# Optimization experiments

Hardware: AMD Instinct MI355X
Metric: run time of the kernel (lower is better)

Reference implementation:

```python
import jax, jax.numpy as jnp
import numpy as np

# model constants (match init_kwargs)
B, T, D = 2, 2048, 2048          # batch, seq_len, d_model (= d_in = d_out)
H, G = 32, 8                     # num_heads, num_kv_groups
HD = D // H                      # head_dim = 64
GROUP = H // G                   # 4 query heads per KV group
ROPE_BASE = 10000.0


def _apply_rope(x):
    # x: (b, heads, t, hd); rotate-half RoPE over absolute positions 0..t-1
    t = x.shape[2]
    half = HD // 2
    inv_freq = 1.0 / (ROPE_BASE ** (jnp.arange(half, dtype=jnp.float32) * 2.0 / HD))
    ang = jnp.arange(t, dtype=jnp.float32)[:, None] * inv_freq[None, :]   # (t, half)
    cos, sin = jnp.cos(ang), jnp.sin(ang)
    x1, x2 = x[..., :half], x[..., half:]
    out = jnp.concatenate([x1 * cos - x2 * sin, x2 * cos + x1 * sin], axis=-1)
    return out.astype(x.dtype)


def setup_inputs() -> dict:
    key = jax.random.key(0)
    kx, kq, kk, kv, ko = jax.random.split(key, 5)
    scale = 0.02
    x = jax.random.normal(kx, (B, T, D), dtype=jnp.float32)
    # linear weights stored as (in, out) so y = x @ W
    Wq = jax.random.normal(kq, (D, D), dtype=jnp.float32) * scale
    Wk = jax.random.normal(kk, (D, G * HD), dtype=jnp.float32) * scale
    Wv = jax.random.normal(kv, (D, G * HD), dtype=jnp.float32) * scale
    Wo = jax.random.normal(ko, (D, D), dtype=jnp.float32) * scale
    return {"x": x, "Wq": Wq, "Wk": Wk, "Wv": Wv, "Wo": Wo}


def reference(x, Wq, Wk, Wv, Wo):
    b, t, _ = x.shape
    q = (x @ Wq).reshape(b, t, H, HD).transpose(0, 2, 1, 3)   # (b, H, t, hd)
    k = (x @ Wk).reshape(b, t, G, HD).transpose(0, 2, 1, 3)   # (b, G, t, hd)
    v = (x @ Wv).reshape(b, t, G, HD).transpose(0, 2, 1, 3)
    q = _apply_rope(q)
    k = _apply_rope(k)
    # GQA: physically duplicate K/V per query-head group (repeat_interleave)
    k = jnp.repeat(k, GROUP, axis=1)                          # (b, H, t, hd)
    v = jnp.repeat(v, GROUP, axis=1)
    scores = jnp.einsum('bhqd,bhkd->bhqk', q, k)              # (b, H, t, t)
    causal = jnp.triu(jnp.ones((t, t), dtype=bool), k=1)
    scores = jnp.where(causal, -jnp.inf, scores)
    attn = jax.nn.softmax(scores / jnp.sqrt(jnp.float32(HD)), axis=-1)
    ctx = jnp.einsum('bhqk,bhkd->bhqd', attn, v)              # (b, H, t, hd)
    # faithful to source: transpose(-2, -1) then reshape (NOT the usual (b,t,H,hd) order)
    ctx = jnp.swapaxes(ctx, -2, -1).reshape(b, t, D)
    return ctx @ Wo
```

## Files before the change

kernel.cpp:

```cpp
#include <hip/hip_runtime.h>

typedef unsigned short u16;
typedef unsigned int u32;
typedef __bf16 bf16x8 __attribute__((ext_vector_type(8)));
typedef float f32x4 __attribute__((ext_vector_type(4)));
typedef u16 u16x8 __attribute__((ext_vector_type(8)));
typedef __attribute__((address_space(1))) const void gvoid;
typedef __attribute__((address_space(3))) void svoid;

#define T_SEQ 2048
#define NEG_INF (-__builtin_huge_valf())

__device__ __forceinline__ u16 f2bf(float f) {
  union { float f; unsigned u; } x; x.f = f;
  unsigned u = x.u;
  return (u16)((u + 0x7FFFu + ((u >> 16) & 1u)) >> 16);
}
__device__ __forceinline__ float bf2f(u16 h) {
  union { unsigned u; float f; } x; x.u = ((unsigned)h) << 16;
  return x.f;
}
__device__ __forceinline__ u32 pack_bf2(float lo, float hi) {
  u32 r;
  asm("v_cvt_pk_bf16_f32 %0, %1, %2" : "=v"(r) : "v"(lo), "v"(hi));
  return r;
}
__device__ __forceinline__ int swz16(int row, int col16) {
  int blk = (col16 >> 3) ^ (row & 7) ^ ((row >> 3) & 7);
  return row * 64 + ((blk & 7) << 3) + (col16 & 7);
}

__global__ __launch_bounds__(256) void cast_f32_bf16(const float* __restrict__ in,
                                                     u16* __restrict__ out, long n) {
  long i = ((long)blockIdx.x * 256 + threadIdx.x) * 4;
  if (i >= n) return;
  float4 v = *(const float4*)(in + i);
  ushort4 o;
  o.x = f2bf(v.x); o.y = f2bf(v.y); o.z = f2bf(v.z); o.w = f2bf(v.w);
  *(ushort4*)(out + i) = o;
}

__global__ __launch_bounds__(256) void transpose_cast(const float* __restrict__ W,
                                                      u16* __restrict__ WT, int K, int N) {
  __shared__ float tile[32][33];
  int nb = blockIdx.x * 32, kb = blockIdx.y * 32;
  int tx = threadIdx.x, ty = threadIdx.y;
  #pragma unroll
  for (int i = 0; i < 32; i += 8)
    tile[ty + i][tx] = W[(size_t)(kb + ty + i) * N + nb + tx];
  __syncthreads();
  #pragma unroll
  for (int i = 0; i < 32; i += 8)
    WT[(size_t)(nb + ty + i) * K + kb + tx] = f2bf(tile[tx][ty + i]);
}

__global__ __launch_bounds__(256) void rope_table_k(float2* __restrict__ tab) {
  int idx = blockIdx.x * 256 + threadIdx.x;
  int t = idx >> 5, d = idx & 31;
  float inv = powf(10000.0f, -(float)d / 32.0f);
  float ang = (float)t * inv;
  float s, c;
  sincosf(ang, &s, &c);
  tab[idx] = make_float2(c, s);
}

__global__ __launch_bounds__(256) void rope_apply_v(u16* __restrict__ X,
                                                    const float2* __restrict__ tab,
                                                    long total, int lsh) {
  long idx = (long)blockIdx.x * 256 + threadIdx.x;
  if (idx >= total) return;
  int row = (int)(idx >> lsh);
  int u = (int)(idx & ((1 << lsh) - 1));
  int h = u >> 2, d0 = (u & 3) << 3;
  int t = row & (T_SEQ - 1);
  int cols = 1 << (lsh + 4);
  u16* p = X + (size_t)row * cols + h * 64 + d0;
  u16x8 lo = *(u16x8*)p;
  u16x8 hi = *(u16x8*)(p + 32);
  const float4* tp = (const float4*)(tab + t * 32 + d0);
  float4 cs0 = tp[0], cs1 = tp[1], cs2 = tp[2], cs3 = tp[3];
  float cbuf[16];
  *(float4*)(cbuf) = cs0; *(float4*)(cbuf + 4) = cs1;
  *(float4*)(cbuf + 8) = cs2; *(float4*)(cbuf + 12) = cs3;
  u16x8 olo, ohi;
  #pragma unroll
  for (int e = 0; e < 8; ++e) {
    float c = cbuf[2 * e], s = cbuf[2 * e + 1];
    float x1 = bf2f(lo[e]), x2 = bf2f(hi[e]);
    olo[e] = f2bf(x1 * c - x2 * s);
    ohi[e] = f2bf(x2 * c + x1 * s);
  }
  *(u16x8*)p = olo;
  *(u16x8*)(p + 32) = ohi;
}

template<int OUT_F32>
__global__ __launch_bounds__(256) void gemm_bt(const u16* __restrict__ A,
                                               const u16* __restrict__ BT,
                                               void* __restrict__ Cout,
                                               int M, int N, int K) {
  __shared__ __align__(16) u16 As[128 * 64];
  __shared__ __align__(16) u16 Bs[128 * 64];
  const int tid = threadIdx.x;
  const int w = tid >> 6, lane = tid & 63;
  const int r16 = lane & 15, kg = lane >> 4;
  const size_t rowBase = (size_t)blockIdx.y * 128;
  const size_t colBase = (size_t)blockIdx.x * 128;
  const int wm = (w >> 1) * 64, wn = (w & 1) * 64;
  f32x4 acc[4][4] = {};

  const u16* Abase = A + (rowBase + w * 32 + (lane >> 3)) * (size_t)K + (lane & 7) * 8;
  const u16* Bbase = BT + (colBase + w * 32 + (lane >> 3)) * (size_t)K + (lane & 7) * 8;

  for (int k0 = 0; k0 < K; k0 += 64) {
    __syncthreads();
    #pragma unroll
    for (int i = 0; i < 4; ++i) {
      __builtin_amdgcn_global_load_lds((gvoid*)(Abase + (size_t)i * 8 * K + k0),
                                       (svoid*)(&As[(w * 32 + i * 8) * 64]), 16, 0, 0);
      __builtin_amdgcn_global_load_lds((gvoid*)(Bbase + (size_t)i * 8 * K + k0),
                                       (svoid*)(&Bs[(w * 32 + i * 8) * 64]), 16, 0, 0);
    }
    __syncthreads();
    #pragma unroll
    for (int kk = 0; kk < 2; ++kk) {
      bf16x8 af[4], bfv[4];
      #pragma unroll
      for (int mi = 0; mi < 4; ++mi)
        af[mi] = *(const bf16x8*)(&As[(wm + mi * 16 + r16) * 64 + kk * 32 + kg * 8]);
      #pragma unroll
      for (int ni = 0; ni < 4; ++ni)
        bfv[ni] = *(const bf16x8*)(&Bs[(wn + ni * 16 + r16) * 64 + kk * 32 + kg * 8]);
      __builtin_amdgcn_s_setprio(1);
      #pragma unroll
      for (int mi = 0; mi < 4; ++mi)
        #pragma unroll
        for (int ni = 0; ni < 4; ++ni)
          acc[mi][ni] = __builtin_amdgcn_mfma_f32_16x16x32_bf16(af[mi], bfv[ni], acc[mi][ni], 0, 0, 0);
      __builtin_amdgcn_s_setprio(0);
    }
  }

  #pragma unroll
  for (int mi = 0; mi < 4; ++mi)
    #pragma unroll
    for (int ni = 0; ni < 4; ++ni) {
      size_t row = rowBase + wm + mi * 16 + kg * 4;
      size_t col = colBase + wn + ni * 16 + r16;
      if (OUT_F32) {
        float* C = (float*)Cout;
        #pragma unroll
        for (int r = 0; r < 4; ++r) C[(row + r) * N + col] = acc[mi][ni][r];
      } else {
        u16* C = (u16*)Cout;
        #pragma unroll
        for (int r = 0; r < 4; ++r) C[(row + r) * N + col] = f2bf(acc[mi][ni][r]);
      }
    }
}

__global__ __launch_bounds__(256) void attn_fwd(const u16* __restrict__ Q,
                                                const u16* __restrict__ Kg,
                                                const u16* __restrict__ Vg,
                                                u16* __restrict__ ctxT) {
  const int bh = blockIdx.x, qt = blockIdx.y;
  const int b = bh >> 5, h = bh & 31, g = h >> 2;
  const int tid = threadIdx.x, w = tid >> 6, lane = tid & 63;
  const int r16 = lane & 15, kg = lane >> 4;
  const int qbase = qt * 128;
  const int wq = qbase + w * 32;

  const u16* Qp = Q + (size_t)b * T_SEQ * 2048 + (size_t)h * 64;
  const u16* Kp = Kg + (size_t)b * T_SEQ * 512 + (size_t)g * 64;
  const u16* Vp = Vg + (size_t)b * T_SEQ * 512 + (size_t)g * 64;

  __shared__ __align__(16) u16 Kt[64 * 64];
  __shared__ __align__(16) u16 Vt[64 * 64];

  bf16x8 qf[2][2];
  #pragma unroll
  for (int mi = 0; mi < 2; ++mi)
    #pragma unroll
    for (int ks = 0; ks < 2; ++ks)
      qf[mi][ks] = *(const bf16x8*)(Qp + (size_t)(wq + mi * 16 + r16) * 2048 + ks * 32 + kg * 8);

  f32x4 acc[4][2] = {};
  float m_i[2] = {NEG_INF, NEG_INF}, l_i[2] = {0.0f, 0.0f};
  const float SCALE = 0.18033688f;

  const int nkt = (qbase + 128) >> 6;
  const int srow = tid >> 3, sc8 = tid & 7;

  for (int kt = 0; kt < nkt; ++kt) {
    const int kvb = kt << 6;
    __syncthreads();
    #pragma unroll
    for (int p = 0; p < 2; ++p) {
      int row = p * 32 + srow;
      bf16x8 kv8 = *(const bf16x8*)(Kp + (size_t)(kvb + row) * 512 + sc8 * 8);
      *(bf16x8*)(&Kt[swz16(row, sc8 * 8)]) = kv8;
    }
    {
      bf16x8 v0 = *(const bf16x8*)(Vp + (size_t)(kvb + 2 * srow) * 512 + sc8 * 8);
      bf16x8 v1 = *(const bf16x8*)(Vp + (size_t)(kvb + 2 * srow + 1) * 512 + sc8 * 8);
      const u16* va = (const u16*)&v0;
      const u16* vb = (const u16*)&v1;
      #pragma unroll
      for (int j = 0; j < 8; ++j) {
        u32 wv = (u32)va[j] | ((u32)vb[j] << 16);
        *(u32*)(&Vt[swz16(sc8 * 8 + j, 2 * srow)]) = wv;
      }
    }
    __syncthreads();
    if (kvb > wq + 31) continue;

    f32x4 st[4][2] = {};
    #pragma unroll
    for (int ks = 0; ks < 2; ++ks) {
      bf16x8 kf[4];
      #pragma unroll
      for (int ni = 0; ni < 4; ++ni)
        kf[ni] = *(const bf16x8*)(&Kt[swz16(ni * 16 + r16, ks * 32 + kg * 8)]);
      __builtin_amdgcn_s_setprio(1);
      #pragma unroll
      for (int ni = 0; ni < 4; ++ni)
        #pragma unroll
        for (int mi = 0; mi < 2; ++mi)
          st[ni][mi] = __builtin_amdgcn_mfma_f32_16x16x32_bf16(kf[ni], qf[mi][ks], st[ni][mi], 0, 0, 0);
      __builtin_amdgcn_s_setprio(0);
    }

    u32 pkk[2][4][2];
    #pragma unroll
    for (int mi = 0; mi < 2; ++mi) {
      const int q = wq + mi * 16 + r16;
      float mx = NEG_INF;
      #pragma unroll
      for (int ni = 0; ni < 4; ++ni)
        #pragma unroll
        for (int r = 0; r < 4; ++r) {
          float v = st[ni][mi][r];
          int kv = kvb + ni * 16 + kg * 4 + r;
          v = (kv <= q) ? v : NEG_INF;
          st[ni][mi][r] = v;
          mx = fmaxf(mx, v);
        }
      mx = fmaxf(mx, __shfl_xor(mx, 16, 64));
      mx = fmaxf(mx, __shfl_xor(mx, 32, 64));
      float mnew = fmaxf(m_i[mi], mx);
      float alpha = exp2f((m_i[mi] - mnew) * SCALE);
      float nm = mnew * SCALE;
      m_i[mi] = mnew;
      float rs = 0.0f;
      #pragma unroll
      for (int ni = 0; ni < 4; ++ni) {
        float p0 = exp2f(fmaf(st[ni][mi][0], SCALE, -nm));
        float p1 = exp2f(fmaf(st[ni][mi][1], SCALE, -nm));
        float p2 = exp2f(fmaf(st[ni][mi][2], SCALE, -nm));
        float p3 = exp2f(fmaf(st[ni][mi][3], SCALE, -nm));
        rs += (p0 + p1) + (p2 + p3);
        pkk[mi][ni][0] = pack_bf2(p0, p1);
        pkk[mi][ni][1] = pack_bf2(p2, p3);
      }
      rs += __shfl_xor(rs, 16, 64);
      rs += __shfl_xor(rs, 32, 64);
      l_i[mi] = l_i[mi] * alpha + rs;
      #pragma unroll
      for (int di = 0; di < 4; ++di)
        #pragma unroll
        for (int r = 0; r < 4; ++r) acc[di][mi][r] *= alpha;
    }

    #pragma unroll
    for (int ks = 0; ks < 2; ++ks) {
      bf16x8 vfr[4];
      #pragma unroll
      for (int di = 0; di < 4; ++di)
        vfr[di] = *(const bf16x8*)(&Vt[swz16(di * 16 + r16, ks * 32 + kg * 8)]);
      const int s0 = ((kg & 1) * 2) * 16 + r16;
      const int s1 = s0 + 16;
      const bool hi = (kg >> 1) != 0;
      #pragma unroll
      for (int mi = 0; mi < 2; ++mi) {
        u32 a0 = __shfl(pkk[mi][2 * ks][0], s0, 64);
        u32 b0 = __shfl(pkk[mi][2 * ks + 1][0], s0, 64);
        u32 a1 = __shfl(pkk[mi][2 * ks][1], s0, 64);
        u32 b1 = __shfl(pkk[mi][2 * ks + 1][1], s0, 64);
        u32 a2 = __shfl(pkk[mi][2 * ks][0], s1, 64);
        u32 b2 = __shfl(pkk[mi][2 * ks + 1][0], s1, 64);
        u32 a3 = __shfl(pkk[mi][2 * ks][1], s1, 64);
        u32 b3 = __shfl(pkk[mi][2 * ks + 1][1], s1, 64);
        union { u32 u[4]; bf16x8 v; } pu;
        pu.u[0] = hi ? b0 : a0;
        pu.u[1] = hi ? b1 : a1;
        pu.u[2] = hi ? b2 : a2;
        pu.u[3] = hi ? b3 : a3;
        __builtin_amdgcn_s_setprio(1);
        #pragma unroll
        for (int di = 0; di < 4; ++di)
          acc[di][mi] = __builtin_amdgcn_mfma_f32_16x16x32_bf16(vfr[di], pu.v, acc[di][mi], 0, 0, 0);
        __builtin_amdgcn_s_setprio(0);
      }
    }
  }

  float inv[2] = {1.0f / l_i[0], 1.0f / l_i[1]};
  #pragma unroll
  for (int di = 0; di < 4; ++di)
    #pragma unroll
    for (int mi = 0; mi < 2; ++mi)
      #pragma unroll
      for (int r = 0; r < 4; ++r) {
        size_t row = (size_t)(b * 2048 + h * 64 + di * 16 + kg * 4 + r);
        ctxT[row * 2048 + wq + mi * 16 + r16] = f2bf(acc[di][mi][r] * inv[mi]);
      }
}

extern "C" void kernel_launch(void* const* d_in, const int* in_sizes, int n_in,
                              void* d_out, int out_size, void* d_ws, size_t ws_size,
                              hipStream_t stream) {
  const float* x  = (const float*)d_in[0];
  const float* Wq = (const float*)d_in[1];
  const float* Wk = (const float*)d_in[2];
  const float* Wv = (const float*)d_in[3];
  const float* Wo = (const float*)d_in[4];
  float* out = (float*)d_out;
  char* ws = (char*)d_ws;

  u16* xb   = (u16*)(ws);
  u16* Qb   = (u16*)(ws + 16777216);
  u16* Kb   = (u16*)(ws + 33554432);
  u16* Vb   = (u16*)(ws + 37748736);
  u16* ctxT = (u16*)(ws + 41943040);
  u16* WqT  = (u16*)(ws + 58720256);
  u16* WkT  = (u16*)(ws + 67108864);
  u16* WvT  = (u16*)(ws + 69206016);
  u16* WoT  = (u16*)(ws + 71303168);
  float2* tab = (float2*)(ws + 79691776);

  cast_f32_bf16<<<8192, 256, 0, stream>>>(x, xb, 8388608L);
  rope_table_k<<<256, 256, 0, stream>>>(tab);
  transpose_cast<<<dim3(64, 64), dim3(32, 8), 0, stream>>>(Wq, WqT, 2048, 2048);
  transpose_cast<<<dim3(16, 64), dim3(32, 8), 0, stream>>>(Wk, WkT, 2048, 512);
  transpose_cast<<<dim3(16, 64), dim3(32, 8), 0, stream>>>(Wv, WvT, 2048, 512);
  transpose_cast<<<dim3(64, 64), dim3(32, 8), 0, stream>>>(Wo, WoT, 2048, 2048);

  gemm_bt<0><<<dim3(16, 32), 256, 0, stream>>>(xb, WqT, Qb, 4096, 2048, 2048);
  gemm_bt<0><<<dim3(4, 32), 256, 0, stream>>>(xb, WkT, Kb, 4096, 512, 2048);
  gemm_bt<0><<<dim3(4, 32), 256, 0, stream>>>(xb, WvT, Vb, 4096, 512, 2048);

  rope_apply_v<<<2048, 256, 0, stream>>>(Qb, tab, 524288L, 7);
  rope_apply_v<<<512, 256, 0, stream>>>(Kb, tab, 131072L, 5);

  attn_fwd<<<dim3(64, 16), 256, 0, stream>>>(Qb, Kb, Vb, ctxT);

  gemm_bt<1><<<dim3(16, 32), 256, 0, stream>>>(ctxT, WoT, out, 4096, 2048, 2048);
}
```

Before: 459.5 us.

## Fuse QKV GEMM with RoPE epilogue and double-buffer attention K/V tiles

Concatenates Wq/Wk/Wv into one transposed weight and runs a single QKV GEMM whose epilogue applies RoPE to the Q and K columns, which removes two GEMM launches and both separate RoPE passes over global memory. The attention kernel now reads from the packed QKV buffer, double-buffers K/V tiles in LDS, loads K with direct global-to-LDS copies, and skips the online-softmax rescale unless the running max grows past a threshold. The lazy rescale changes numerics slightly, and the double buffers double the LDS footprint, which may lower occupancy.

```diff
diff --git a/kernel.cpp b/kernel.cpp
--- a/kernel.cpp
+++ b/kernel.cpp
@@ -64,41 +64,12 @@
   tab[idx] = make_float2(c, s);
 }
 
-__global__ __launch_bounds__(256) void rope_apply_v(u16* __restrict__ X,
-                                                    const float2* __restrict__ tab,
-                                                    long total, int lsh) {
-  long idx = (long)blockIdx.x * 256 + threadIdx.x;
-  if (idx >= total) return;
-  int row = (int)(idx >> lsh);
-  int u = (int)(idx & ((1 << lsh) - 1));
-  int h = u >> 2, d0 = (u & 3) << 3;
-  int t = row & (T_SEQ - 1);
-  int cols = 1 << (lsh + 4);
-  u16* p = X + (size_t)row * cols + h * 64 + d0;
-  u16x8 lo = *(u16x8*)p;
-  u16x8 hi = *(u16x8*)(p + 32);
-  const float4* tp = (const float4*)(tab + t * 32 + d0);
-  float4 cs0 = tp[0], cs1 = tp[1], cs2 = tp[2], cs3 = tp[3];
-  float cbuf[16];
-  *(float4*)(cbuf) = cs0; *(float4*)(cbuf + 4) = cs1;
-  *(float4*)(cbuf + 8) = cs2; *(float4*)(cbuf + 12) = cs3;
-  u16x8 olo, ohi;
-  #pragma unroll
-  for (int e = 0; e < 8; ++e) {
-    float c = cbuf[2 * e], s = cbuf[2 * e + 1];
-    float x1 = bf2f(lo[e]), x2 = bf2f(hi[e]);
-    olo[e] = f2bf(x1 * c - x2 * s);
-    ohi[e] = f2bf(x2 * c + x1 * s);
-  }
-  *(u16x8*)p = olo;
-  *(u16x8*)(p + 32) = ohi;
-}
-
-template<int OUT_F32>
+template<int MODE>
 __global__ __launch_bounds__(256) void gemm_bt(const u16* __restrict__ A,
                                                const u16* __restrict__ BT,
                                                void* __restrict__ Cout,
-                                               int M, int N, int K) {
+                                               int M, int N, int K,
+                                               const float2* __restrict__ tab) {
   __shared__ __align__(16) u16 As[128 * 64];
   __shared__ __align__(16) u16 Bs[128 * 64];
   const int tid = threadIdx.x;
@@ -141,13 +112,30 @@
     }
   }
 
+  if (MODE == 2 && colBase < 2560) {
+    #pragma unroll
+    for (int mi = 0; mi < 4; ++mi)
+      #pragma unroll
+      for (int p = 0; p < 2; ++p) {
+        int d = (wn + p * 16 + r16) & 63;
+        #pragma unroll
+        for (int r = 0; r < 4; ++r) {
+          int t = (int)((rowBase + wm + mi * 16 + kg * 4 + r) & (T_SEQ - 1));
+          float2 cs = tab[t * 32 + d];
+          float x1 = acc[mi][p][r], x2 = acc[mi][p + 2][r];
+          acc[mi][p][r]     = x1 * cs.x - x2 * cs.y;
+          acc[mi][p + 2][r] = x2 * cs.x + x1 * cs.y;
+        }
+      }
+  }
+
   #pragma unroll
   for (int mi = 0; mi < 4; ++mi)
     #pragma unroll
     for (int ni = 0; ni < 4; ++ni) {
       size_t row = rowBase + wm + mi * 16 + kg * 4;
       size_t col = colBase + wn + ni * 16 + r16;
-      if (OUT_F32) {
+      if (MODE == 1) {
         float* C = (float*)Cout;
         #pragma unroll
         for (int r = 0; r < 4; ++r) C[(row + r) * N + col] = acc[mi][ni][r];
@@ -159,30 +147,28 @@
     }
 }
 
-__global__ __launch_bounds__(256) void attn_fwd(const u16* __restrict__ Q,
-                                                const u16* __restrict__ Kg,
-                                                const u16* __restrict__ Vg,
+__global__ __launch_bounds__(256) void attn_fwd(const u16* __restrict__ QKV,
                                                 u16* __restrict__ ctxT) {
   const int bh = blockIdx.x, qt = blockIdx.y;
   const int b = bh >> 5, h = bh & 31, g = h >> 2;
   const int tid = threadIdx.x, w = tid >> 6, lane = tid & 63;
   const int r16 = lane & 15, kg = lane >> 4;
-  const int qbase = qt * 128;
-  const int wq = qbase + w * 32;
-
-  const u16* Qp = Q + (size_t)b * T_SEQ * 2048 + (size_t)h * 64;
-  const u16* Kp = Kg + (size_t)b * T_SEQ * 512 + (size_t)g * 64;
-  const u16* Vp = Vg + (size_t)b * T_SEQ * 512 + (size_t)g * 64;
-
-  __shared__ __align__(16) u16 Kt[64 * 64];
-  __shared__ __align__(16) u16 Vt[64 * 64];
+  const int qbase = qt * 128, wq = qbase + w * 32;
+  const int LD = 3072;
+
+  const u16* Qp = QKV + (size_t)b * T_SEQ * LD + h * 64;
+  const u16* Kp = QKV + (size_t)b * T_SEQ * LD + 2048 + g * 64;
+  const u16* Vp = QKV + (size_t)b * T_SEQ * LD + 2560 + g * 64;
+
+  __shared__ __align__(16) u16 Kt[2][64 * 64];
+  __shared__ __align__(16) u16 Vt[2][64 * 64];
 
   bf16x8 qf[2][2];
   #pragma unroll
   for (int mi = 0; mi < 2; ++mi)
     #pragma unroll
     for (int ks = 0; ks < 2; ++ks)
-      qf[mi][ks] = *(const bf16x8*)(Qp + (size_t)(wq + mi * 16 + r16) * 2048 + ks * 32 + kg * 8);
+      qf[mi][ks] = *(const bf16x8*)(Qp + (size_t)(wq + mi * 16 + r16) * LD + ks * 32 + kg * 8);
 
   f32x4 acc[4][2] = {};
   float m_i[2] = {NEG_INF, NEG_INF}, l_i[2] = {0.0f, 0.0f};
@@ -190,118 +176,163 @@
 
   const int nkt = (qbase + 128) >> 6;
   const int srow = tid >> 3, sc8 = tid & 7;
+  const int klr = (lane >> 3);
+  const int kblk = lane & 7;
+
+  {
+    #pragma unroll
+    for (int i = 0; i < 2; ++i) {
+      int lr = w * 16 + i * 8 + klr;
+      int sb = kblk ^ ((lr & 7) ^ ((lr >> 3) & 7));
+      __builtin_amdgcn_global_load_lds((gvoid*)(Kp + (size_t)lr * LD + sb * 8),
+                                       (svoid*)(&Kt[0][(w * 16 + i * 8) * 64]), 16, 0, 0);
+    }
+    bf16x8 v0 = *(const bf16x8*)(Vp + (size_t)(2 * srow) * LD + sc8 * 8);
+    bf16x8 v1 = *(const bf16x8*)(Vp + (size_t)(2 * srow + 1) * LD + sc8 * 8);
+    const u16* va = (const u16*)&v0;
+    const u16* vb = (const u16*)&v1;
+    #pragma unroll
+    for (int j = 0; j < 8; ++j)
+      *(u32*)(&Vt[0][swz16(sc8 * 8 + j, 2 * srow)]) = (u32)va[j] | ((u32)vb[j] << 16);
+    __syncthreads();
+  }
 
   for (int kt = 0; kt < nkt; ++kt) {
     const int kvb = kt << 6;
-    __syncthreads();
-    #pragma unroll
-    for (int p = 0; p < 2; ++p) {
-      int row = p * 32 + srow;
-      bf16x8 kv8 = *(const bf16x8*)(Kp + (size_t)(kvb + row) * 512 + sc8 * 8);
-      *(bf16x8*)(&Kt[swz16(row, sc8 * 8)]) = kv8;
-    }
-    {
-      bf16x8 v0 = *(const bf16x8*)(Vp + (size_t)(kvb + 2 * srow) * 512 + sc8 * 8);
-      bf16x8 v1 = *(const bf16x8*)(Vp + (size_t)(kvb + 2 * srow + 1) * 512 + sc8 * 8);
+    const int cur = kt & 1;
+    const bool st = (kt + 1 < nkt);
+    bf16x8 v0, v1;
+    if (st) {
+      #pragma unroll
+      for (int i = 0; i < 2; ++i) {
+        int lr = w * 16 + i * 8 + klr;
+        int sb = kblk ^ ((lr & 7) ^ ((lr >> 3) & 7));
+        __builtin_amdgcn_global_load_lds((gvoid*)(Kp + (size_t)(kvb + 64 + lr) * LD + sb * 8),
+                                         (svoid*)(&Kt[cur ^ 1][(w * 16 + i * 8) * 64]), 16, 0, 0);
+      }
+      v0 = *(const bf16x8*)(Vp + (size_t)(kvb + 64 + 2 * srow) * LD + sc8 * 8);
+      v1 = *(const bf16x8*)(Vp + (size_t)(kvb + 64 + 2 * srow + 1) * LD + sc8 * 8);
+    }
+
+    if (kvb <= wq + 31) {
+      f32x4 stv[4][2] = {};
+      #pragma unroll
+      for (int ks = 0; ks < 2; ++ks) {
+        bf16x8 kf[4];
+        #pragma unroll
+        for (int ni = 0; ni < 4; ++ni)
+          kf[ni] = *(const bf16x8*)(&Kt[cur][swz16(ni * 16 + r16, ks * 32 + kg * 8)]);
+        __builtin_amdgcn_s_setprio(1);
+        #pragma unroll
+        for (int ni = 0; ni < 4; ++ni)
+          #pragma unroll
+          for (int mi = 0; mi < 2; ++mi)
+            stv[ni][mi] = __builtin_amdgcn_mfma_f32_16x16x32_bf16(kf[ni], qf[mi][ks], stv[ni][mi], 0, 0, 0);
+        __builtin_amdgcn_s_setprio(0);
+      }
+
+      if (kvb + 63 > wq) {
+        #pragma unroll
+        for (int mi = 0; mi < 2; ++mi) {
+          const int q = wq + mi * 16 + r16;
+          #pragma unroll
+          for (int ni = 0; ni < 4; ++ni)
+            #pragma unroll
+            for (int r = 0; r < 4; ++r) {
+              int kv = kvb + ni * 16 + kg * 4 + r;
+              if (kv > q) stv[ni][mi][r] = NEG_INF;
+            }
+        }
+      }
+
+      float tmx[2];
+      #pragma unroll
+      for (int mi = 0; mi < 2; ++mi) {
+        float pm = NEG_INF;
+        #pragma unroll
+        for (int ni = 0; ni < 4; ++ni)
+          #pragma unroll
+          for (int r = 0; r < 4; ++r) pm = fmaxf(pm, stv[ni][mi][r]);
+        pm = fmaxf(pm, __shfl_xor(pm, 16, 64));
+        pm = fmaxf(pm, __shfl_xor(pm, 32, 64));
+        tmx[mi] = pm;
+      }
+      bool upd = ((tmx[0] - m_i[0]) * SCALE > 8.0f) || ((tmx[1] - m_i[1]) * SCALE > 8.0f);
+      if (__any(upd)) {
+        #pragma unroll
+        for (int mi = 0; mi < 2; ++mi) {
+          float mnew = fmaxf(m_i[mi], tmx[mi]);
+          float alpha = exp2f((m_i[mi] - mnew) * SCALE);
+          m_i[mi] = mnew;
+          l_i[mi] *= alpha;
+          #pragma unroll
+          for (int di = 0; di < 4; ++di)
+            #pragma unroll
+            for (int r = 0; r < 4; ++r) acc[di][mi][r] *= alpha;
+        }
+      }
+
+      u32 pkk[2][4][2];
+      #pragma unroll
+      for (int mi = 0; mi < 2; ++mi) {
+        float nm = m_i[mi] * SCALE;
+        float rs = 0.0f;
+        #pragma unroll
+        for (int ni = 0; ni < 4; ++ni) {
+          float p0 = exp2f(fmaf(stv[ni][mi][0], SCALE, -nm));
+          float p1 = exp2f(fmaf(stv[ni][mi][1], SCALE, -nm));
+          float p2 = exp2f(fmaf(stv[ni][mi][2], SCALE, -nm));
+          float p3 = exp2f(fmaf(stv[ni][mi][3], SCALE, -nm));
+          rs += (p0 + p1) + (p2 + p3);
+          pkk[mi][ni][0] = pack_bf2(p0, p1);
+          pkk[mi][ni][1] = pack_bf2(p2, p3);
+        }
+        rs += __shfl_xor(rs, 16, 64);
+        rs += __shfl_xor(rs, 32, 64);
+        l_i[mi] += rs;
+      }
+
+      #pragma unroll
+      for (int ks = 0; ks < 2; ++ks) {
+        bf16x8 vfr[4];
+        #pragma unroll
+        for (int di = 0; di < 4; ++di)
+          vfr[di] = *(const bf16x8*)(&Vt[cur][swz16(di * 16 + r16, ks * 32 + kg * 8)]);
+        const int s0 = (kg & 1) * 32 + r16;
+        const int s1 = s0 + 16;
+        const bool hi = (kg >> 1) != 0;
+        #pragma unroll
+        for (int mi = 0; mi < 2; ++mi) {
+          u32 a0 = __shfl(pkk[mi][2 * ks][0], s0, 64);
+          u32 b0 = __shfl(pkk[mi][2 * ks + 1][0], s0, 64);
+          u32 a1 = __shfl(pkk[mi][2 * ks][1], s0, 64);
+          u32 b1 = __shfl(pkk[mi][2 * ks + 1][1], s0, 64);
+          u32 a2 = __shfl(pkk[mi][2 * ks][0], s1, 64);
+          u32 b2 = __shfl(pkk[mi][2 * ks + 1][0], s1, 64);
+          u32 a3 = __shfl(pkk[mi][2 * ks][1], s1, 64);
+          u32 b3 = __shfl(pkk[mi][2 * ks + 1][1], s1, 64);
+          union { u32 u[4]; bf16x8 v; } pu;
+          pu.u[0] = hi ? b0 : a0;
+          pu.u[1] = hi ? b1 : a1;
+          pu.u[2] = hi ? b2 : a2;
+          pu.u[3] = hi ? b3 : a3;
+          __builtin_amdgcn_s_setprio(1);
+          #pragma unroll
+          for (int di = 0; di < 4; ++di)
+            acc[di][mi] = __builtin_amdgcn_mfma_f32_16x16x32_bf16(vfr[di], pu.v, acc[di][mi], 0, 0, 0);
+          __builtin_amdgcn_s_setprio(0);
+        }
+      }
+    }
+
+    if (st) {
       const u16* va = (const u16*)&v0;
       const u16* vb = (const u16*)&v1;
       #pragma unroll
-      for (int j = 0; j < 8; ++j) {
-        u32 wv = (u32)va[j] | ((u32)vb[j] << 16);
-        *(u32*)(&Vt[swz16(sc8 * 8 + j, 2 * srow)]) = wv;
-      }
+      for (int j = 0; j < 8; ++j)
+        *(u32*)(&Vt[cur ^ 1][swz16(sc8 * 8 + j, 2 * srow)]) = (u32)va[j] | ((u32)vb[j] << 16);
     }
     __syncthreads();
-    if (kvb > wq + 31) continue;
-
-    f32x4 st[4][2] = {};
-    #pragma unroll
-    for (int ks = 0; ks < 2; ++ks) {
-      bf16x8 kf[4];
-      #pragma unroll
-      for (int ni = 0; ni < 4; ++ni)
-        kf[ni] = *(const bf16x8*)(&Kt[swz16(ni * 16 + r16, ks * 32 + kg * 8)]);
-      __builtin_amdgcn_s_setprio(1);
-      #pragma unroll
-      for (int ni = 0; ni < 4; ++ni)
-        #pragma unroll
-        for (int mi = 0; mi < 2; ++mi)
-          st[ni][mi] = __builtin_amdgcn_mfma_f32_16x16x32_bf16(kf[ni], qf[mi][ks], st[ni][mi], 0, 0, 0);
-      __builtin_amdgcn_s_setprio(0);
-    }
-
-    u32 pkk[2][4][2];
-    #pragma unroll
-    for (int mi = 0; mi < 2; ++mi) {
-      const int q = wq + mi * 16 + r16;
-      float mx = NEG_INF;
-      #pragma unroll
-      for (int ni = 0; ni < 4; ++ni)
-        #pragma unroll
-        for (int r = 0; r < 4; ++r) {
-          float v = st[ni][mi][r];
-          int kv = kvb + ni * 16 + kg * 4 + r;
-          v = (kv <= q) ? v : NEG_INF;
-          st[ni][mi][r] = v;
-          mx = fmaxf(mx, v);
-        }
-      mx = fmaxf(mx, __shfl_xor(mx, 16, 64));
-      mx = fmaxf(mx, __shfl_xor(mx, 32, 64));
-      float mnew = fmaxf(m_i[mi], mx);
-      float alpha = exp2f((m_i[mi] - mnew) * SCALE);
-      float nm = mnew * SCALE;
-      m_i[mi] = mnew;
-      float rs = 0.0f;
-      #pragma unroll
-      for (int ni = 0; ni < 4; ++ni) {
-        float p0 = exp2f(fmaf(st[ni][mi][0], SCALE, -nm));
-        float p1 = exp2f(fmaf(st[ni][mi][1], SCALE, -nm));
-        float p2 = exp2f(fmaf(st[ni][mi][2], SCALE, -nm));
-        float p3 = exp2f(fmaf(st[ni][mi][3], SCALE, -nm));
-        rs += (p0 + p1) + (p2 + p3);
-        pkk[mi][ni][0] = pack_bf2(p0, p1);
-        pkk[mi][ni][1] = pack_bf2(p2, p3);
-      }
-      rs += __shfl_xor(rs, 16, 64);
-      rs += __shfl_xor(rs, 32, 64);
-      l_i[mi] = l_i[mi] * alpha + rs;
-      #pragma unroll
-      for (int di = 0; di < 4; ++di)
-        #pragma unroll
-        for (int r = 0; r < 4; ++r) acc[di][mi][r] *= alpha;
-    }
-
-    #pragma unroll
-    for (int ks = 0; ks < 2; ++ks) {
-      bf16x8 vfr[4];
-      #pragma unroll
-      for (int di = 0; di < 4; ++di)
-        vfr[di] = *(const bf16x8*)(&Vt[swz16(di * 16 + r16, ks * 32 + kg * 8)]);
-      const int s0 = ((kg & 1) * 2) * 16 + r16;
-      const int s1 = s0 + 16;
-      const bool hi = (kg >> 1) != 0;
-      #pragma unroll
-      for (int mi = 0; mi < 2; ++mi) {
-        u32 a0 = __shfl(pkk[mi][2 * ks][0], s0, 64);
-        u32 b0 = __shfl(pkk[mi][2 * ks + 1][0], s0, 64);
-        u32 a1 = __shfl(pkk[mi][2 * ks][1], s0, 64);
-        u32 b1 = __shfl(pkk[mi][2 * ks + 1][1], s0, 64);
-        u32 a2 = __shfl(pkk[mi][2 * ks][0], s1, 64);
-        u32 b2 = __shfl(pkk[mi][2 * ks + 1][0], s1, 64);
-        u32 a3 = __shfl(pkk[mi][2 * ks][1], s1, 64);
-        u32 b3 = __shfl(pkk[mi][2 * ks + 1][1], s1, 64);
-        union { u32 u[4]; bf16x8 v; } pu;
-        pu.u[0] = hi ? b0 : a0;
-        pu.u[1] = hi ? b1 : a1;
-        pu.u[2] = hi ? b2 : a2;
-        pu.u[3] = hi ? b3 : a3;
-        __builtin_amdgcn_s_setprio(1);
-        #pragma unroll
-        for (int di = 0; di < 4; ++di)
-          acc[di][mi] = __builtin_amdgcn_mfma_f32_16x16x32_bf16(vfr[di], pu.v, acc[di][mi], 0, 0, 0);
-        __builtin_amdgcn_s_setprio(0);
-      }
-    }
   }
 
   float inv[2] = {1.0f / l_i[0], 1.0f / l_i[1]};
@@ -327,32 +358,23 @@
   float* out = (float*)d_out;
   char* ws = (char*)d_ws;
 
-  u16* xb   = (u16*)(ws);
-  u16* Qb   = (u16*)(ws + 16777216);
-  u16* Kb   = (u16*)(ws + 33554432);
-  u16* Vb   = (u16*)(ws + 37748736);
-  u16* ctxT = (u16*)(ws + 41943040);
-  u16* WqT  = (u16*)(ws + 58720256);
-  u16* WkT  = (u16*)(ws + 67108864);
-  u16* WvT  = (u16*)(ws + 69206016);
-  u16* WoT  = (u16*)(ws + 71303168);
+  u16* xb     = (u16*)(ws);
+  u16* QKVb   = (u16*)(ws + 16777216);
+  u16* ctxT   = (u16*)(ws + 41943040);
+  u16* WqkvT  = (u16*)(ws + 58720256);
+  u16* WoT    = (u16*)(ws + 71303168);
   float2* tab = (float2*)(ws + 79691776);
 
   cast_f32_bf16<<<8192, 256, 0, stream>>>(x, xb, 8388608L);
   rope_table_k<<<256, 256, 0, stream>>>(tab);
-  transpose_cast<<<dim3(64, 64), dim3(32, 8), 0, stream>>>(Wq, WqT, 2048, 2048);
-  transpose_cast<<<dim3(16, 64), dim3(32, 8), 0, stream>>>(Wk, WkT, 2048, 512);
-  transpose_cast<<<dim3(16, 64), dim3(32, 8), 0, stream>>>(Wv, WvT, 2048, 512);
+  transpose_cast<<<dim3(64, 64), dim3(32, 8), 0, stream>>>(Wq, WqkvT, 2048, 2048);
+  transpose_cast<<<dim3(16, 64), dim3(32, 8), 0, stream>>>(Wk, WqkvT + 2048L * 2048, 2048, 512);
+  transpose_cast<<<dim3(16, 64), dim3(32, 8), 0, stream>>>(Wv, WqkvT + 2560L * 2048, 2048, 512);
   transpose_cast<<<dim3(64, 64), dim3(32, 8), 0, stream>>>(Wo, WoT, 2048, 2048);
 
-  gemm_bt<0><<<dim3(16, 32), 256, 0, stream>>>(xb, WqT, Qb, 4096, 2048, 2048);
-  gemm_bt<0><<<dim3(4, 32), 256, 0, stream>>>(xb, WkT, Kb, 4096, 512, 2048);
-  gemm_bt<0><<<dim3(4, 32), 256, 0, stream>>>(xb, WvT, Vb, 4096, 512, 2048);
-
-  rope_apply_v<<<2048, 256, 0, stream>>>(Qb, tab, 524288L, 7);
-  rope_apply_v<<<512, 256, 0, stream>>>(Kb, tab, 131072L, 5);
-
-  attn_fwd<<<dim3(64, 16), 256, 0, stream>>>(Qb, Kb, Vb, ctxT);
-
-  gemm_bt<1><<<dim3(16, 32), 256, 0, stream>>>(ctxT, WoT, out, 4096, 2048, 2048);
-}
+  gemm_bt<2><<<dim3(24, 32), 256, 0, stream>>>(xb, WqkvT, QKVb, 4096, 3072, 2048, tab);
+
+  attn_fwd<<<dim3(64, 16), 256, 0, stream>>>(QKVb, ctxT);
+
+  gemm_bt<1><<<dim3(16, 32), 256, 0, stream>>>(ctxT, WoT, out, 4096, 2048, 2048, nullptr);
+}
```

Result: faster. 398.8 us (-13.2%).
